# Kernel optimization log

Measured on AMD Instinct MI355X. Metric: run time of the kernel, lower is better.

The kernel has to match this reference:

```python
import jax, jax.numpy as jnp
import numpy as np

C_M, C_Z, C = 256, 128, 32
LN_EPS = 1e-5


def setup_inputs() -> dict:
    key = jax.random.key(0)
    ks = jax.random.split(key, 9)
    S, R = 128, 384  # N_seq, N_res
    m = jax.random.normal(ks[0], (S, R, C_M), dtype=jnp.float32)
    ln_g = jnp.ones((C_M,), jnp.float32)
    ln_b = jnp.zeros((C_M,), jnp.float32)
    w1 = jax.random.normal(ks[1], (C_M, C), jnp.float32) / np.sqrt(C_M)
    b1 = jnp.zeros((C,), jnp.float32)
    w2 = jax.random.normal(ks[2], (C_M, C), jnp.float32) / np.sqrt(C_M)
    b2 = jnp.zeros((C,), jnp.float32)
    w_out = jax.random.normal(ks[3], (C * C, C_Z), jnp.float32) / np.sqrt(C * C)
    b_out = jnp.zeros((C_Z,), jnp.float32)
    return {"m": m, "ln_g": ln_g, "ln_b": ln_b, "w1": w1, "b1": b1,
            "w2": w2, "b2": b2, "w_out": w_out, "b_out": b_out}


def reference(m, ln_g, ln_b, w1, b1, w2, b2, w_out, b_out):
    S, R, _ = m.shape
    # LayerNorm over c_m
    mu = jnp.mean(m, axis=-1, keepdims=True)
    var = jnp.var(m, axis=-1, keepdims=True)
    mn = (m - mu) * jax.lax.rsqrt(var + LN_EPS) * ln_g + ln_b
    a = mn @ w1 + b1  # (S, R, c)
    b = mn @ w2 + b2  # (S, R, c)
    # outer product summed over N_seq: out[i,j,x,y] = sum_s a[s,i,x] b[s,j,y]
    o = jnp.einsum('six,sjy->ijxy', a, b)  # (R, R, c, c)
    o = o.reshape(R, R, C * C) @ w_out + b_out  # (R, R, c_z)
    return o / S
```

## Files before the change

### kernel.cpp

```cpp
#include <hip/hip_runtime.h>
#include <hip/hip_bf16.h>

#define R_RES 384
#define S_SEQ 128
#define CM 256
#define CC 32
#define CZ 128

typedef __attribute__((ext_vector_type(8))) short bf16x8;
typedef __attribute__((ext_vector_type(4))) float f32x4;
typedef __attribute__((ext_vector_type(16))) float f32x16;
typedef __attribute__((ext_vector_type(4))) int i32x4;

__device__ __forceinline__ short tobf16(float f) {
    union { __hip_bfloat16 h; short s; } u;
    u.h = __float2bfloat16(f);
    return u.s;
}

__global__ void k_transpose_wout(const float* __restrict__ w_out, short* __restrict__ wbTf) {
    __shared__ float t[64][65];
    int k0 = blockIdx.x * 64;
    int z0 = blockIdx.y * 64;
    int tid = threadIdx.x;
    int c = tid & 63, rg = tid >> 6;
#pragma unroll
    for (int rr = 0; rr < 16; ++rr) {
        int kk = rg * 16 + rr;
        t[kk][c] = w_out[(size_t)(k0 + kk) * CZ + z0 + c];
    }
    __syncthreads();
#pragma unroll
    for (int l = 0; l < 2; ++l) {
        int id = l * 256 + tid;
        int f = id >> 6;
        int ksl = f >> 1, fzl = f & 1;
        int ln = id & 63;
        int zl = fzl * 32 + (ln & 31);
        int kl = ksl * 16 + (ln >> 5) * 8;
        bf16x8 pk;
#pragma unroll
        for (int j = 0; j < 8; ++j) pk[j] = tobf16(t[kl + j][zl]);
        size_t fz = blockIdx.y * 2 + fzl;
        size_t ks16 = blockIdx.x * 4 + ksl;
        *(bf16x8*)(wbTf + ((fz * 64 + ks16) * 64 + ln) * 8) = pk;
    }
}

__global__ void k_pack_w12(const float* __restrict__ w1, const float* __restrict__ w2,
                           short* __restrict__ wcT) {
    int idx = blockIdx.x * 256 + threadIdx.x;
    int k = idx >> 6, n = idx & 63;
    float v = (n < 32) ? w1[k * CC + n] : w2[k * CC + (n - 32)];
    wcT[n * CM + k] = tobf16(v);
}

__global__ __launch_bounds__(256) void k_ln_proj(
    const float* __restrict__ M, const float* __restrict__ ln_g, const float* __restrict__ ln_b,
    const float* __restrict__ b1, const float* __restrict__ b2,
    const short* __restrict__ wcT, short* __restrict__ aTf, short* __restrict__ bTf) {
    __shared__ short mnb[64 * 256];
    __shared__ short ab_s[2][32 * 72];
    int r = blockIdx.x >> 1;
    int s0 = (blockIdx.x & 1) * 64;
    int tid = threadIdx.x, lane = tid & 63, w = tid >> 6;
    int g = lane >> 4, r16 = lane & 15;
    float4 gv = *(const float4*)(ln_g + lane * 4);
    float4 bv = *(const float4*)(ln_b + lane * 4);
    for (int it = 0; it < 16; ++it) {
        int sl = it * 4 + w;
        float4 v = *(const float4*)(M + ((size_t)(s0 + sl) * R_RES + r) * CM + lane * 4);
        float sum = v.x + v.y + v.z + v.w;
        float sq = v.x * v.x + v.y * v.y + v.z * v.z + v.w * v.w;
#pragma unroll
        for (int off = 32; off; off >>= 1) {
            sum += __shfl_xor(sum, off);
            sq  += __shfl_xor(sq, off);
        }
        float mu = sum * (1.0f / 256.0f);
        float var = sq * (1.0f / 256.0f) - mu * mu;
        float rstd = rsqrtf(var + 1e-5f);
        short4 mnp;
        mnp.x = tobf16((v.x - mu) * rstd * gv.x + bv.x);
        mnp.y = tobf16((v.y - mu) * rstd * gv.y + bv.y);
        mnp.z = tobf16((v.z - mu) * rstd * gv.z + bv.z);
        mnp.w = tobf16((v.w - mu) * rstd * gv.w + bv.w);
        int byte = sl * 512 + lane * 8;
        byte ^= ((sl & 7) << 4);
        *(short4*)((char*)mnb + byte) = mnp;
    }
    __syncthreads();
    f32x4 acc[4] = {{0,0,0,0},{0,0,0,0},{0,0,0,0},{0,0,0,0}};
    int srow = w * 16 + r16;
#pragma unroll
    for (int ks = 0; ks < 8; ++ks) {
        int byte = srow * 512 + ks * 64 + g * 16;
        byte ^= ((srow & 7) << 4);
        bf16x8 af = *(const bf16x8*)((const char*)mnb + byte);
#pragma unroll
        for (int nt = 0; nt < 4; ++nt) {
            bf16x8 bf = *(const bf16x8*)(wcT + (nt * 16 + r16) * CM + ks * 32 + g * 8);
            acc[nt] = __builtin_amdgcn_mfma_f32_16x16x32_bf16(af, bf, acc[nt], 0, 0, 0);
        }
    }
#pragma unroll
    for (int nt = 0; nt < 4; ++nt) {
        int n = nt * 16 + r16;
        int x = n & 31, sel = n >> 5;
        float bias = sel ? b2[x] : b1[x];
#pragma unroll
        for (int rr = 0; rr < 4; ++rr) {
            int sl = w * 16 + g * 4 + rr;
            ab_s[sel][x * 72 + sl] = tobf16(acc[nt][rr] + bias);
        }
    }
    __syncthreads();
    int piece = tid >> 6;
    int fl = piece >> 1, kl = piece & 1;
    int ln = tid & 63;
    int x = fl * 16 + (ln & 15);
    int s_loc = kl * 32 + (ln >> 4) * 8;
    i32x4 va = *(const i32x4*)((const char*)ab_s[0] + (x * 72 + s_loc) * 2);
    i32x4 vb = *(const i32x4*)((const char*)ab_s[1] + (x * 72 + s_loc) * 2);
    size_t off = ((((size_t)r * 2 + fl) * 4 + (s0 >> 5) + kl) * 64 + ln) * 16;
    *(i32x4*)((char*)aTf + off) = va;
    *(i32x4*)((char*)bTf + off) = vb;
}

__global__ __launch_bounds__(512, 4) void k_opm(
    const short* __restrict__ aTf, const short* __restrict__ bTf,
    const short* __restrict__ wbTf, const float* __restrict__ b_out,
    float* __restrict__ out) {
    __shared__ __align__(16) char smem[65536];
    int tid = threadIdx.x, lane = tid & 63, w = tid >> 6;
    int g = lane >> 4, r16 = lane & 15;
    int l32 = lane & 31, h = lane >> 5;
    int wm = w & 3, wn = w >> 2;
    int bj = blockIdx.x, bi = blockIdx.y;

    const char* gB = (const char*)bTf + (size_t)bj * 32768;
#pragma unroll
    for (int it = 0; it < 4; ++it) {
        int q = it * 8192 + tid * 16;
        __builtin_amdgcn_global_load_lds(
            (const __attribute__((address_space(1))) void*)(gB + q),
            (__attribute__((address_space(3))) void*)(smem + q), 16, 0, 0);
    }
    __syncthreads();

    f32x4 acc[4][4] = {};
    const char* gA = (const char*)aTf + ((size_t)bi * 16 + wm * 4) * 4096;
#pragma unroll
    for (int ks = 0; ks < 4; ++ks) {
        bf16x8 bf[4], af[4];
#pragma unroll
        for (int ni = 0; ni < 4; ++ni)
            bf[ni] = *(const bf16x8*)(smem + (((wn * 4 + ni) * 4 + ks) * 64 + lane) * 16);
#pragma unroll
        for (int mi = 0; mi < 4; ++mi)
            af[mi] = *(const bf16x8*)(gA + ((mi * 4 + ks) * 64 + lane) * 16);
        __builtin_amdgcn_s_setprio(1);
#pragma unroll
        for (int mi = 0; mi < 4; ++mi)
#pragma unroll
            for (int ni = 0; ni < 4; ++ni)
                acc[mi][ni] = __builtin_amdgcn_mfma_f32_16x16x32_bf16(bf[ni], af[mi], acc[mi][ni], 0, 0, 0);
        __builtin_amdgcn_s_setprio(0);
    }
    __syncthreads();

#pragma unroll
    for (int mi = 0; mi < 4; ++mi)
#pragma unroll
        for (int ni = 0; ni < 4; ++ni) {
            int m = wm * 64 + mi * 16 + r16;
            int nb = wn * 64 + ni * 16 + g * 4;
            int i = m >> 5, x = m & 31;
            int j = nb >> 5, y0 = nb & 31;
            int p = i * 4 + j;
            int byte = (p * 2048 + x * 64 + y0 * 2) ^ (((p & 7) ^ (x & 7)) << 4);
            short4 pk;
            pk.x = tobf16(acc[mi][ni][0]);
            pk.y = tobf16(acc[mi][ni][1]);
            pk.z = tobf16(acc[mi][ni][2]);
            pk.w = tobf16(acc[mi][ni][3]);
            *(short4*)(smem + byte) = pk;
        }
    __syncthreads();

    int kh = w & 1, zq = w >> 1;
    f32x16 c2a = {0,0,0,0,0,0,0,0,0,0,0,0,0,0,0,0};
    f32x16 c2b = {0,0,0,0,0,0,0,0,0,0,0,0,0,0,0,0};
    const short* wbase = wbTf + (size_t)((zq * 64 + kh * 32) * 64) * 8;
#pragma unroll 8
    for (int ks = 0; ks < 32; ++ks) {
        int x = (kh * 32 + ks) >> 1;
        int byte = (l32 * 2048 + kh * 1024 + ks * 32 + h * 16) ^ ((((l32 & 7) ^ (x & 7))) << 4);
        bf16x8 a2f = *(const bf16x8*)(smem + byte);
        bf16x8 wbf = *(const bf16x8*)(wbase + (ks * 64 + lane) * 8);
        if (ks & 1) c2b = __builtin_amdgcn_mfma_f32_32x32x16_bf16(a2f, wbf, c2b, 0, 0, 0);
        else        c2a = __builtin_amdgcn_mfma_f32_32x32x16_bf16(a2f, wbf, c2a, 0, 0, 0);
    }
    f32x16 c2 = c2a + c2b;
    __syncthreads();

#pragma unroll
    for (int q = 0; q < 4; ++q) {
        f32x4 v;
        v[0] = c2[q * 4 + 0]; v[1] = c2[q * 4 + 1];
        v[2] = c2[q * 4 + 2]; v[3] = c2[q * 4 + 3];
        int byte = ((zq * 2 + kh) * 4096 + l32 * 128 + q * 32 + h * 16) ^ ((l32 & 7) << 4);
        *(f32x4*)(smem + byte) = v;
    }
    __syncthreads();

    int z = tid & 127, zq2 = z >> 5, zp = z & 31;
    int pr0 = tid >> 7;
    float bo = b_out[z];
#pragma unroll
    for (int stp = 0; stp < 2; ++stp) {
        int prq = pr0 + stp * 4;
        int base = zq2 * 8192 + zp * 128 + prq * 16;
        int sw = (zp & 7) << 4;
        f32x4 v0 = *(const f32x4*)(smem + (base ^ sw));
        f32x4 v1 = *(const f32x4*)(smem + ((base + 4096) ^ sw));
#pragma unroll
        for (int rr = 0; rr < 4; ++rr) {
            int p = prq * 4 + rr;
            int ig = bi * 8 + (p >> 2);
            int jg = bj * 4 + (p & 3);
            out[((size_t)ig * R_RES + jg) * CZ + z] = (v0[rr] + v1[rr] + bo) * (1.0f / 128.0f);
        }
    }
}

extern "C" void kernel_launch(void* const* d_in, const int* in_sizes, int n_in,
                              void* d_out, int out_size, void* d_ws, size_t ws_size,
                              hipStream_t stream) {
    const float* M     = (const float*)d_in[0];
    const float* ln_g  = (const float*)d_in[1];
    const float* ln_b  = (const float*)d_in[2];
    const float* w1    = (const float*)d_in[3];
    const float* b1    = (const float*)d_in[4];
    const float* w2    = (const float*)d_in[5];
    const float* b2    = (const float*)d_in[6];
    const float* w_out = (const float*)d_in[7];
    const float* b_out = (const float*)d_in[8];
    float* out = (float*)d_out;

    short* aTf  = (short*)d_ws;
    short* bTf  = aTf + 12288 * 128;
    short* wbTf = bTf + 12288 * 128;
    short* wcT  = wbTf + 128 * 1024;

    k_transpose_wout<<<dim3(16, 2), 256, 0, stream>>>(w_out, wbTf);
    k_pack_w12<<<64, 256, 0, stream>>>(w1, w2, wcT);
    k_ln_proj<<<768, 256, 0, stream>>>(M, ln_g, ln_b, b1, b2, wcT, aTf, bTf);
    k_opm<<<dim3(96, 48), 512, 0, stream>>>(aTf, bTf, wbTf, b_out, out);
}
```

Measured before the change: 133.8 us.

## Double outer-product block tile to 8x8 residue pairs with A staged in LDS

Each k_opm block now computes an 8x8 tile of residue pairs with 1024 threads and 128KB of LDS, instead of 8x4 with 512 threads. Both the A and B projections are staged into LDS with global_load_lds, so A is no longer read straight from global memory. Halving the block count halves the number of times the full W_out slice is streamed from L2 per output pair. The epilogue is also rewritten so each thread writes two vectorized float4 stores. The cost is a very large LDS footprint, likely one block per CU, and extra register pressure from the 1024-thread launch bounds.

Measured after the change: 143.6 us. +7.3%, slower.

```diff
diff --git a/kernel.cpp b/kernel.cpp
--- a/kernel.cpp
+++ b/kernel.cpp
@@ -127,38 +127,41 @@
     *(i32x4*)((char*)bTf + off) = vb;
 }
 
-__global__ __launch_bounds__(512, 4) void k_opm(
+__global__ __launch_bounds__(1024, 4) void k_opm(
     const short* __restrict__ aTf, const short* __restrict__ bTf,
     const short* __restrict__ wbTf, const float* __restrict__ b_out,
     float* __restrict__ out) {
-    __shared__ __align__(16) char smem[65536];
+    __shared__ __align__(16) char smem[131072];
     int tid = threadIdx.x, lane = tid & 63, w = tid >> 6;
     int g = lane >> 4, r16 = lane & 15;
     int l32 = lane & 31, h = lane >> 5;
     int wm = w & 3, wn = w >> 2;
     int bj = blockIdx.x, bi = blockIdx.y;
 
-    const char* gB = (const char*)bTf + (size_t)bj * 32768;
+    const char* gA = (const char*)aTf + (size_t)bi * 65536;
+    const char* gB = (const char*)bTf + (size_t)bj * 65536;
 #pragma unroll
     for (int it = 0; it < 4; ++it) {
-        int q = it * 8192 + tid * 16;
+        int q = it * 16384 + tid * 16;
+        __builtin_amdgcn_global_load_lds(
+            (const __attribute__((address_space(1))) void*)(gA + q),
+            (__attribute__((address_space(3))) void*)(smem + q), 16, 0, 0);
         __builtin_amdgcn_global_load_lds(
             (const __attribute__((address_space(1))) void*)(gB + q),
-            (__attribute__((address_space(3))) void*)(smem + q), 16, 0, 0);
+            (__attribute__((address_space(3))) void*)(smem + 65536 + q), 16, 0, 0);
     }
     __syncthreads();
 
     f32x4 acc[4][4] = {};
-    const char* gA = (const char*)aTf + ((size_t)bi * 16 + wm * 4) * 4096;
 #pragma unroll
     for (int ks = 0; ks < 4; ++ks) {
         bf16x8 bf[4], af[4];
 #pragma unroll
         for (int ni = 0; ni < 4; ++ni)
-            bf[ni] = *(const bf16x8*)(smem + (((wn * 4 + ni) * 4 + ks) * 64 + lane) * 16);
+            bf[ni] = *(const bf16x8*)(smem + 65536 + (((wn * 4 + ni) * 4 + ks) * 64 + lane) * 16);
 #pragma unroll
         for (int mi = 0; mi < 4; ++mi)
-            af[mi] = *(const bf16x8*)(gA + ((mi * 4 + ks) * 64 + lane) * 16);
+            af[mi] = *(const bf16x8*)(smem + (((wm * 4 + mi) * 4 + ks) * 64 + lane) * 16);
         __builtin_amdgcn_s_setprio(1);
 #pragma unroll
         for (int mi = 0; mi < 4; ++mi)
@@ -177,7 +180,7 @@
             int nb = wn * 64 + ni * 16 + g * 4;
             int i = m >> 5, x = m & 31;
             int j = nb >> 5, y0 = nb & 31;
-            int p = i * 4 + j;
+            int p = i * 8 + j;
             int byte = (p * 2048 + x * 64 + y0 * 2) ^ (((p & 7) ^ (x & 7)) << 4);
             short4 pk;
             pk.x = tobf16(acc[mi][ni][0]);
@@ -188,14 +191,16 @@
         }
     __syncthreads();
 
-    int kh = w & 1, zq = w >> 1;
+    int kh = w & 1, zq = (w >> 1) & 3, pd = w >> 3;
     f32x16 c2a = {0,0,0,0,0,0,0,0,0,0,0,0,0,0,0,0};
     f32x16 c2b = {0,0,0,0,0,0,0,0,0,0,0,0,0,0,0,0};
     const short* wbase = wbTf + (size_t)((zq * 64 + kh * 32) * 64) * 8;
+    int pbase = pd * 32 + l32;
 #pragma unroll 8
     for (int ks = 0; ks < 32; ++ks) {
-        int x = (kh * 32 + ks) >> 1;
-        int byte = (l32 * 2048 + kh * 1024 + ks * 32 + h * 16) ^ ((((l32 & 7) ^ (x & 7))) << 4);
+        int x = kh * 16 + (ks >> 1);
+        int byte = (pbase * 2048 + kh * 1024 + ks * 32 + h * 16)
+                   ^ ((((l32 & 7) ^ (x & 7))) << 4);
         bf16x8 a2f = *(const bf16x8*)(smem + byte);
         bf16x8 wbf = *(const bf16x8*)(wbase + (ks * 64 + lane) * 8);
         if (ks & 1) c2b = __builtin_amdgcn_mfma_f32_32x32x16_bf16(a2f, wbf, c2b, 0, 0, 0);
@@ -205,32 +210,41 @@
     __syncthreads();
 
 #pragma unroll
-    for (int q = 0; q < 4; ++q) {
-        f32x4 v;
-        v[0] = c2[q * 4 + 0]; v[1] = c2[q * 4 + 1];
-        v[2] = c2[q * 4 + 2]; v[3] = c2[q * 4 + 3];
-        int byte = ((zq * 2 + kh) * 4096 + l32 * 128 + q * 32 + h * 16) ^ ((l32 & 7) << 4);
-        *(f32x4*)(smem + byte) = v;
-    }
-    __syncthreads();
-
-    int z = tid & 127, zq2 = z >> 5, zp = z & 31;
-    int pr0 = tid >> 7;
-    float bo = b_out[z];
-#pragma unroll
-    for (int stp = 0; stp < 2; ++stp) {
-        int prq = pr0 + stp * 4;
-        int base = zq2 * 8192 + zp * 128 + prq * 16;
-        int sw = (zp & 7) << 4;
-        f32x4 v0 = *(const f32x4*)(smem + (base ^ sw));
-        f32x4 v1 = *(const f32x4*)(smem + ((base + 4096) ^ sw));
+    for (int q = 0; q < 4; ++q)
 #pragma unroll
         for (int rr = 0; rr < 4; ++rr) {
-            int p = prq * 4 + rr;
-            int ig = bi * 8 + (p >> 2);
-            int jg = bj * 4 + (p & 3);
-            out[((size_t)ig * R_RES + jg) * CZ + z] = (v0[rr] + v1[rr] + bo) * (1.0f / 128.0f);
-        }
+            int prow = pd * 32 + q * 8 + h * 4 + rr;
+            int zz = zq * 32 + l32;
+            int byte = (kh * 32768 + prow * 512 + zz * 4) ^ ((prow & 1) << 4);
+            *(float*)(smem + byte) = c2[q * 4 + rr];
+        }
+    __syncthreads();
+
+    {
+        int p = tid >> 4;
+        int zo = (tid & 15) * 8;
+        int sw = (p & 1) << 4;
+        int base = p * 512 + zo * 4;
+        f32x4 u0 = *(const f32x4*)(smem + ((base) ^ sw));
+        f32x4 u1 = *(const f32x4*)(smem + ((base + 16) ^ sw));
+        f32x4 v0 = *(const f32x4*)(smem + ((base + 32768) ^ sw));
+        f32x4 v1 = *(const f32x4*)(smem + ((base + 16 + 32768) ^ sw));
+        float4 bo0 = *(const float4*)(b_out + zo);
+        float4 bo1 = *(const float4*)(b_out + zo + 4);
+        f32x4 r0, r1;
+        r0[0] = (u0[0] + v0[0] + bo0.x) * (1.0f / 128.0f);
+        r0[1] = (u0[1] + v0[1] + bo0.y) * (1.0f / 128.0f);
+        r0[2] = (u0[2] + v0[2] + bo0.z) * (1.0f / 128.0f);
+        r0[3] = (u0[3] + v0[3] + bo0.w) * (1.0f / 128.0f);
+        r1[0] = (u1[0] + v1[0] + bo1.x) * (1.0f / 128.0f);
+        r1[1] = (u1[1] + v1[1] + bo1.y) * (1.0f / 128.0f);
+        r1[2] = (u1[2] + v1[2] + bo1.z) * (1.0f / 128.0f);
+        r1[3] = (u1[3] + v1[3] + bo1.w) * (1.0f / 128.0f);
+        int ig = bi * 8 + (p >> 3);
+        int jg = bj * 8 + (p & 7);
+        float* po = out + ((size_t)ig * R_RES + jg) * CZ + zo;
+        *(f32x4*)(po) = r0;
+        *(f32x4*)(po + 4) = r1;
     }
 }
 
@@ -256,5 +270,5 @@
     k_transpose_wout<<<dim3(16, 2), 256, 0, stream>>>(w_out, wbTf);
     k_pack_w12<<<64, 256, 0, stream>>>(w1, w2, wcT);
     k_ln_proj<<<768, 256, 0, stream>>>(M, ln_g, ln_b, b1, b2, wcT, aTf, bTf);
-    k_opm<<<dim3(96, 48), 512, 0, stream>>>(aTf, bTf, wbTf, b_out, out);
-}
+    k_opm<<<dim3(48, 48), 1024, 0, stream>>>(aTf, bTf, wbTf, b_out, out);
+}
```

## Remap OPM warp tiling, prefetch A and W fragments, use lgkm-only barriers

Applied to the files above, without the earlier changes.

The outer-product stage now has each warp own one full i row (2x8 MFMA tiles) instead of a 4x4 tile, so each warp reuses two A fragments across all eight B fragments. A fragments are prefetched one k-step ahead from global memory. W_out fragments for the second GEMM are software-pipelined four steps ahead, with their first loads issued before the barrier. The __syncthreads calls become lgkmcnt-only waits plus s_barrier, and one barrier between the accumulator dump and the second GEMM is merged with the prefetch. The gains depend on the compiler keeping outstanding vmem loads correctly ordered; register pressure also rises.

Result: faster. 128.1 us (-4.3%).

```diff
diff --git a/kernel.cpp b/kernel.cpp
--- a/kernel.cpp
+++ b/kernel.cpp
@@ -16,6 +16,12 @@
     union { __hip_bfloat16 h; short s; } u;
     u.h = __float2bfloat16(f);
     return u.s;
+}
+
+__device__ __forceinline__ void lgkm_barrier() {
+    asm volatile("s_waitcnt lgkmcnt(0)" ::: "memory");
+    __builtin_amdgcn_s_barrier();
+    __builtin_amdgcn_sched_barrier(0);
 }
 
 __global__ void k_transpose_wout(const float* __restrict__ w_out, short* __restrict__ wbTf) {
@@ -135,7 +141,7 @@
     int tid = threadIdx.x, lane = tid & 63, w = tid >> 6;
     int g = lane >> 4, r16 = lane & 15;
     int l32 = lane & 31, h = lane >> 5;
-    int wm = w & 3, wn = w >> 2;
+    int wm = w;
     int bj = blockIdx.x, bi = blockIdx.y;
 
     const char* gB = (const char*)bTf + (size_t)bj * 32768;
@@ -146,38 +152,51 @@
             (const __attribute__((address_space(1))) void*)(gB + q),
             (__attribute__((address_space(3))) void*)(smem + q), 16, 0, 0);
     }
-    __syncthreads();
-
-    f32x4 acc[4][4] = {};
-    const char* gA = (const char*)aTf + ((size_t)bi * 16 + wm * 4) * 4096;
+    const char* gA = (const char*)aTf + (size_t)bi * 65536;
+    bf16x8 afc0 = *(const bf16x8*)(gA + (((wm * 2 + 0) * 4 + 0) * 64 + lane) * 16);
+    bf16x8 afc1 = *(const bf16x8*)(gA + (((wm * 2 + 1) * 4 + 0) * 64 + lane) * 16);
+    __syncthreads();
+
+    f32x4 acc[2][8] = {};
 #pragma unroll
     for (int ks = 0; ks < 4; ++ks) {
-        bf16x8 bf[4], af[4];
+        int ksn = (ks + 1) & 3;
+        bf16x8 bf[8];
 #pragma unroll
         for (int ni = 0; ni < 4; ++ni)
-            bf[ni] = *(const bf16x8*)(smem + (((wn * 4 + ni) * 4 + ks) * 64 + lane) * 16);
-#pragma unroll
-        for (int mi = 0; mi < 4; ++mi)
-            af[mi] = *(const bf16x8*)(gA + ((mi * 4 + ks) * 64 + lane) * 16);
+            bf[ni] = *(const bf16x8*)(smem + ((ni * 4 + ks) * 64 + lane) * 16);
+        bf16x8 afn0 = *(const bf16x8*)(gA + (((wm * 2 + 0) * 4 + ksn) * 64 + lane) * 16);
+        bf16x8 afn1 = *(const bf16x8*)(gA + (((wm * 2 + 1) * 4 + ksn) * 64 + lane) * 16);
         __builtin_amdgcn_s_setprio(1);
 #pragma unroll
-        for (int mi = 0; mi < 4; ++mi)
-#pragma unroll
-            for (int ni = 0; ni < 4; ++ni)
-                acc[mi][ni] = __builtin_amdgcn_mfma_f32_16x16x32_bf16(bf[ni], af[mi], acc[mi][ni], 0, 0, 0);
+        for (int ni = 0; ni < 4; ++ni) {
+            acc[0][ni] = __builtin_amdgcn_mfma_f32_16x16x32_bf16(bf[ni], afc0, acc[0][ni], 0, 0, 0);
+            acc[1][ni] = __builtin_amdgcn_mfma_f32_16x16x32_bf16(bf[ni], afc1, acc[1][ni], 0, 0, 0);
+        }
         __builtin_amdgcn_s_setprio(0);
-    }
-    __syncthreads();
-
-#pragma unroll
-    for (int mi = 0; mi < 4; ++mi)
-#pragma unroll
-        for (int ni = 0; ni < 4; ++ni) {
-            int m = wm * 64 + mi * 16 + r16;
-            int nb = wn * 64 + ni * 16 + g * 4;
-            int i = m >> 5, x = m & 31;
+#pragma unroll
+        for (int ni = 4; ni < 8; ++ni)
+            bf[ni] = *(const bf16x8*)(smem + ((ni * 4 + ks) * 64 + lane) * 16);
+        __builtin_amdgcn_s_setprio(1);
+#pragma unroll
+        for (int ni = 4; ni < 8; ++ni) {
+            acc[0][ni] = __builtin_amdgcn_mfma_f32_16x16x32_bf16(bf[ni], afc0, acc[0][ni], 0, 0, 0);
+            acc[1][ni] = __builtin_amdgcn_mfma_f32_16x16x32_bf16(bf[ni], afc1, acc[1][ni], 0, 0, 0);
+        }
+        __builtin_amdgcn_s_setprio(0);
+        afc0 = afn0;
+        afc1 = afn1;
+    }
+    lgkm_barrier();
+
+#pragma unroll
+    for (int mi = 0; mi < 2; ++mi)
+#pragma unroll
+        for (int ni = 0; ni < 8; ++ni) {
+            int x = mi * 16 + r16;
+            int nb = ni * 16 + g * 4;
             int j = nb >> 5, y0 = nb & 31;
-            int p = i * 4 + j;
+            int p = wm * 4 + j;
             int byte = (p * 2048 + x * 64 + y0 * 2) ^ (((p & 7) ^ (x & 7)) << 4);
             short4 pk;
             pk.x = tobf16(acc[mi][ni][0]);
@@ -186,23 +205,43 @@
             pk.w = tobf16(acc[mi][ni][3]);
             *(short4*)(smem + byte) = pk;
         }
-    __syncthreads();
 
     int kh = w & 1, zq = w >> 1;
+    const short* wbase = wbTf + (size_t)((zq * 64 + kh * 32) * 64) * 8;
+    bf16x8 wpf[4];
+#pragma unroll
+    for (int u = 0; u < 4; ++u)
+        wpf[u] = *(const bf16x8*)(wbase + (u * 64 + lane) * 8);
+    lgkm_barrier();
+
     f32x16 c2a = {0,0,0,0,0,0,0,0,0,0,0,0,0,0,0,0};
     f32x16 c2b = {0,0,0,0,0,0,0,0,0,0,0,0,0,0,0,0};
-    const short* wbase = wbTf + (size_t)((zq * 64 + kh * 32) * 64) * 8;
-#pragma unroll 8
-    for (int ks = 0; ks < 32; ++ks) {
-        int x = (kh * 32 + ks) >> 1;
-        int byte = (l32 * 2048 + kh * 1024 + ks * 32 + h * 16) ^ ((((l32 & 7) ^ (x & 7))) << 4);
-        bf16x8 a2f = *(const bf16x8*)(smem + byte);
-        bf16x8 wbf = *(const bf16x8*)(wbase + (ks * 64 + lane) * 8);
-        if (ks & 1) c2b = __builtin_amdgcn_mfma_f32_32x32x16_bf16(a2f, wbf, c2b, 0, 0, 0);
-        else        c2a = __builtin_amdgcn_mfma_f32_32x32x16_bf16(a2f, wbf, c2a, 0, 0, 0);
+#pragma unroll
+    for (int kq = 0; kq < 8; ++kq) {
+        bf16x8 w0 = wpf[0], w1 = wpf[1], w2 = wpf[2], w3 = wpf[3];
+        if (kq < 7) {
+#pragma unroll
+            for (int u = 0; u < 4; ++u)
+                wpf[u] = *(const bf16x8*)(wbase + ((kq * 4 + 4 + u) * 64 + lane) * 8);
+        }
+        bf16x8 a2f[4];
+#pragma unroll
+        for (int u = 0; u < 4; ++u) {
+            int ks = kq * 4 + u;
+            int x = (kh * 32 + ks) >> 1;
+            int byte = (l32 * 2048 + kh * 1024 + ks * 32 + h * 16)
+                       ^ ((((l32 & 7) ^ (x & 7))) << 4);
+            a2f[u] = *(const bf16x8*)(smem + byte);
+        }
+        __builtin_amdgcn_s_setprio(1);
+        c2a = __builtin_amdgcn_mfma_f32_32x32x16_bf16(a2f[0], w0, c2a, 0, 0, 0);
+        c2b = __builtin_amdgcn_mfma_f32_32x32x16_bf16(a2f[1], w1, c2b, 0, 0, 0);
+        c2a = __builtin_amdgcn_mfma_f32_32x32x16_bf16(a2f[2], w2, c2a, 0, 0, 0);
+        c2b = __builtin_amdgcn_mfma_f32_32x32x16_bf16(a2f[3], w3, c2b, 0, 0, 0);
+        __builtin_amdgcn_s_setprio(0);
     }
     f32x16 c2 = c2a + c2b;
-    __syncthreads();
+    lgkm_barrier();
 
 #pragma unroll
     for (int q = 0; q < 4; ++q) {
@@ -212,7 +251,7 @@
         int byte = ((zq * 2 + kh) * 4096 + l32 * 128 + q * 32 + h * 16) ^ ((l32 & 7) << 4);
         *(f32x4*)(smem + byte) = v;
     }
-    __syncthreads();
+    lgkm_barrier();
 
     int z = tid & 127, zq2 = z >> 5, zp = z & 31;
     int pr0 = tid >> 7;
```

## Make OPM kernel persistent with register-resident w_out and prefetched B tiles

Applied to the files above, without the earlier changes.

Replaces the 96x48 grid with 512 persistent blocks that each process 18 output tiles of 4x4 residue pairs. Each block keeps its w_out slice in registers across all tiles. It prefetches the next B tile into LDS and the next A fragment while the current tile finishes. The w_out packing layout is changed to match 16x16x32 MFMAs in the second GEMM. The goal is to amortise weight loads and launch overhead and to overlap global loads with compute, at the cost of heavy register use (32 bf16x8 weights per thread), more LDS, and smaller per-tile work with extra barriers.

Measured after the change: 409.8 us. 3.06x slower.

```diff
diff --git a/kernel.cpp b/kernel.cpp
--- a/kernel.cpp
+++ b/kernel.cpp
@@ -9,13 +9,18 @@
 
 typedef __attribute__((ext_vector_type(8))) short bf16x8;
 typedef __attribute__((ext_vector_type(4))) float f32x4;
-typedef __attribute__((ext_vector_type(16))) float f32x16;
 typedef __attribute__((ext_vector_type(4))) int i32x4;
 
 __device__ __forceinline__ short tobf16(float f) {
     union { __hip_bfloat16 h; short s; } u;
     u.h = __float2bfloat16(f);
     return u.s;
+}
+
+__device__ __forceinline__ void lgkm_barrier() {
+    asm volatile("s_waitcnt lgkmcnt(0)" ::: "memory");
+    __builtin_amdgcn_s_barrier();
+    __builtin_amdgcn_sched_barrier(0);
 }
 
 __global__ void k_transpose_wout(const float* __restrict__ w_out, short* __restrict__ wbTf) {
@@ -34,16 +39,16 @@
     for (int l = 0; l < 2; ++l) {
         int id = l * 256 + tid;
         int f = id >> 6;
-        int ksl = f >> 1, fzl = f & 1;
+        int z16l = f >> 1, k32l = f & 1;
         int ln = id & 63;
-        int zl = fzl * 32 + (ln & 31);
-        int kl = ksl * 16 + (ln >> 5) * 8;
+        int zl = z16l * 16 + (ln & 15);
+        int kl = k32l * 32 + (ln >> 4) * 8;
         bf16x8 pk;
 #pragma unroll
         for (int j = 0; j < 8; ++j) pk[j] = tobf16(t[kl + j][zl]);
-        size_t fz = blockIdx.y * 2 + fzl;
-        size_t ks16 = blockIdx.x * 4 + ksl;
-        *(bf16x8*)(wbTf + ((fz * 64 + ks16) * 64 + ln) * 8) = pk;
+        int z16 = blockIdx.y * 4 + z16l;
+        int k32 = blockIdx.x * 2 + k32l;
+        *(bf16x8*)(wbTf + ((size_t)(z16 * 32 + k32) * 64 + ln) * 8) = pk;
     }
 }
 
@@ -131,106 +136,123 @@
     const short* __restrict__ aTf, const short* __restrict__ bTf,
     const short* __restrict__ wbTf, const float* __restrict__ b_out,
     float* __restrict__ out) {
-    __shared__ __align__(16) char smem[65536];
+    __shared__ __align__(16) char smem[81920];
     int tid = threadIdx.x, lane = tid & 63, w = tid >> 6;
     int g = lane >> 4, r16 = lane & 15;
-    int l32 = lane & 31, h = lane >> 5;
-    int wm = w & 3, wn = w >> 2;
-    int bj = blockIdx.x, bi = blockIdx.y;
-
-    const char* gB = (const char*)bTf + (size_t)bj * 32768;
-#pragma unroll
-    for (int it = 0; it < 4; ++it) {
-        int q = it * 8192 + tid * 16;
-        __builtin_amdgcn_global_load_lds(
-            (const __attribute__((address_space(1))) void*)(gB + q),
-            (__attribute__((address_space(3))) void*)(smem + q), 16, 0, 0);
-    }
-    __syncthreads();
-
-    f32x4 acc[4][4] = {};
-    const char* gA = (const char*)aTf + ((size_t)bi * 16 + wm * 4) * 4096;
-#pragma unroll
-    for (int ks = 0; ks < 4; ++ks) {
-        bf16x8 bf[4], af[4];
-#pragma unroll
-        for (int ni = 0; ni < 4; ++ni)
-            bf[ni] = *(const bf16x8*)(smem + (((wn * 4 + ni) * 4 + ks) * 64 + lane) * 16);
-#pragma unroll
-        for (int mi = 0; mi < 4; ++mi)
-            af[mi] = *(const bf16x8*)(gA + ((mi * 4 + ks) * 64 + lane) * 16);
-        __builtin_amdgcn_s_setprio(1);
-#pragma unroll
-        for (int mi = 0; mi < 4; ++mi)
-#pragma unroll
-            for (int ni = 0; ni < 4; ++ni)
-                acc[mi][ni] = __builtin_amdgcn_mfma_f32_16x16x32_bf16(bf[ni], af[mi], acc[mi][ni], 0, 0, 0);
-        __builtin_amdgcn_s_setprio(0);
-    }
-    __syncthreads();
-
-#pragma unroll
-    for (int mi = 0; mi < 4; ++mi)
-#pragma unroll
-        for (int ni = 0; ni < 4; ++ni) {
-            int m = wm * 64 + mi * 16 + r16;
-            int nb = wn * 64 + ni * 16 + g * 4;
-            int i = m >> 5, x = m & 31;
-            int j = nb >> 5, y0 = nb & 31;
-            int p = i * 4 + j;
+    int wm = w;
+    int kh = w & 1, zq = w >> 1;
+
+    bf16x8 wb[2][16];
+#pragma unroll
+    for (int zt = 0; zt < 2; ++zt)
+#pragma unroll
+        for (int ks2 = 0; ks2 < 16; ++ks2)
+            wb[zt][ks2] = *(const bf16x8*)(wbTf +
+                (((size_t)(zq * 2 + zt) * 32 + kh * 16 + ks2) * 64 + lane) * 8);
+
+    int pR = tid >> 5;
+    int zR = (tid & 31) * 4;
+    float4 bo4 = *(const float4*)(b_out + zR);
+
+    int t0 = blockIdx.x * 18;
+    const char* Ab = (const char*)aTf;
+    const char* Bb = (const char*)bTf;
+
+    {
+        const char* gB = Bb + (size_t)(t0 % 96) * 32768;
+#pragma unroll
+        for (int q = 0; q < 4; ++q)
+            __builtin_amdgcn_global_load_lds(
+                (const __attribute__((address_space(1))) void*)(gB + q * 8192 + tid * 16),
+                (__attribute__((address_space(3))) void*)(smem + q * 8192 + tid * 16), 16, 0, 0);
+    }
+    bf16x8 afc = *(const bf16x8*)(Ab + ((size_t)((t0 / 96) * 8 + wm) * 4 + 0) * 1024 + lane * 16);
+    asm volatile("s_waitcnt vmcnt(0)" ::: "memory");
+    __syncthreads();
+
+    for (int it = 0; it < 18; ++it) {
+        int t = t0 + it;
+        int bi = t / 96, bj = t % 96;
+        int tn = (it < 17) ? t + 1 : t0;
+        const char* gAc = Ab + (size_t)(bi * 8 + wm) * 4096;
+        const char* gAn = Ab + (size_t)((tn / 96) * 8 + wm) * 4096;
+
+        f32x4 acc[8] = {};
+#pragma unroll
+        for (int ks = 0; ks < 4; ++ks) {
+            bf16x8 bf[8];
+#pragma unroll
+            for (int ni = 0; ni < 8; ++ni)
+                bf[ni] = *(const bf16x8*)(smem + ((ni * 4 + ks) * 64 + lane) * 16);
+            bf16x8 afn = (ks < 3)
+                ? *(const bf16x8*)(gAc + (ks + 1) * 1024 + lane * 16)
+                : *(const bf16x8*)(gAn + lane * 16);
+            __builtin_amdgcn_s_setprio(1);
+#pragma unroll
+            for (int ni = 0; ni < 8; ++ni)
+                acc[ni] = __builtin_amdgcn_mfma_f32_16x16x32_bf16(bf[ni], afc, acc[ni], 0, 0, 0);
+            __builtin_amdgcn_s_setprio(0);
+            afc = afn;
+        }
+        lgkm_barrier();
+
+        if (it < 17) {
+            const char* gB = Bb + (size_t)(tn % 96) * 32768;
+#pragma unroll
+            for (int q = 0; q < 4; ++q)
+                __builtin_amdgcn_global_load_lds(
+                    (const __attribute__((address_space(1))) void*)(gB + q * 8192 + tid * 16),
+                    (__attribute__((address_space(3))) void*)(smem + q * 8192 + tid * 16), 16, 0, 0);
+        }
+
+#pragma unroll
+        for (int ni = 0; ni < 8; ++ni) {
+            int x = (wm & 1) * 16 + r16;
+            int p = (wm >> 1) * 4 + (ni >> 1);
+            int y0 = (ni & 1) * 16 + g * 4;
             int byte = (p * 2048 + x * 64 + y0 * 2) ^ (((p & 7) ^ (x & 7)) << 4);
             short4 pk;
-            pk.x = tobf16(acc[mi][ni][0]);
-            pk.y = tobf16(acc[mi][ni][1]);
-            pk.z = tobf16(acc[mi][ni][2]);
-            pk.w = tobf16(acc[mi][ni][3]);
-            *(short4*)(smem + byte) = pk;
-        }
-    __syncthreads();
-
-    int kh = w & 1, zq = w >> 1;
-    f32x16 c2a = {0,0,0,0,0,0,0,0,0,0,0,0,0,0,0,0};
-    f32x16 c2b = {0,0,0,0,0,0,0,0,0,0,0,0,0,0,0,0};
-    const short* wbase = wbTf + (size_t)((zq * 64 + kh * 32) * 64) * 8;
-#pragma unroll 8
-    for (int ks = 0; ks < 32; ++ks) {
-        int x = (kh * 32 + ks) >> 1;
-        int byte = (l32 * 2048 + kh * 1024 + ks * 32 + h * 16) ^ ((((l32 & 7) ^ (x & 7))) << 4);
-        bf16x8 a2f = *(const bf16x8*)(smem + byte);
-        bf16x8 wbf = *(const bf16x8*)(wbase + (ks * 64 + lane) * 8);
-        if (ks & 1) c2b = __builtin_amdgcn_mfma_f32_32x32x16_bf16(a2f, wbf, c2b, 0, 0, 0);
-        else        c2a = __builtin_amdgcn_mfma_f32_32x32x16_bf16(a2f, wbf, c2a, 0, 0, 0);
-    }
-    f32x16 c2 = c2a + c2b;
-    __syncthreads();
-
-#pragma unroll
-    for (int q = 0; q < 4; ++q) {
-        f32x4 v;
-        v[0] = c2[q * 4 + 0]; v[1] = c2[q * 4 + 1];
-        v[2] = c2[q * 4 + 2]; v[3] = c2[q * 4 + 3];
-        int byte = ((zq * 2 + kh) * 4096 + l32 * 128 + q * 32 + h * 16) ^ ((l32 & 7) << 4);
-        *(f32x4*)(smem + byte) = v;
-    }
-    __syncthreads();
-
-    int z = tid & 127, zq2 = z >> 5, zp = z & 31;
-    int pr0 = tid >> 7;
-    float bo = b_out[z];
-#pragma unroll
-    for (int stp = 0; stp < 2; ++stp) {
-        int prq = pr0 + stp * 4;
-        int base = zq2 * 8192 + zp * 128 + prq * 16;
-        int sw = (zp & 7) << 4;
-        f32x4 v0 = *(const f32x4*)(smem + (base ^ sw));
-        f32x4 v1 = *(const f32x4*)(smem + ((base + 4096) ^ sw));
-#pragma unroll
-        for (int rr = 0; rr < 4; ++rr) {
-            int p = prq * 4 + rr;
-            int ig = bi * 8 + (p >> 2);
-            int jg = bj * 4 + (p & 3);
-            out[((size_t)ig * R_RES + jg) * CZ + z] = (v0[rr] + v1[rr] + bo) * (1.0f / 128.0f);
-        }
+            pk.x = tobf16(acc[ni][0]);
+            pk.y = tobf16(acc[ni][1]);
+            pk.z = tobf16(acc[ni][2]);
+            pk.w = tobf16(acc[ni][3]);
+            *(short4*)(smem + 32768 + byte) = pk;
+        }
+        lgkm_barrier();
+
+        f32x4 c0 = {0,0,0,0}, c1 = {0,0,0,0};
+#pragma unroll
+        for (int ks2 = 0; ks2 < 16; ++ks2) {
+            int x = kh * 16 + ks2;
+            int abyte = (r16 * 2048 + x * 64 + g * 16) ^ ((((r16 & 7) ^ (x & 7))) << 4);
+            bf16x8 a2f = *(const bf16x8*)(smem + 32768 + abyte);
+            c0 = __builtin_amdgcn_mfma_f32_16x16x32_bf16(wb[0][ks2], a2f, c0, 0, 0, 0);
+            c1 = __builtin_amdgcn_mfma_f32_16x16x32_bf16(wb[1][ks2], a2f, c1, 0, 0, 0);
+        }
+        {
+            int b0 = (kh * 8192 + r16 * 512 + (zq * 32 + g * 4) * 4) ^ ((r16 & 7) << 4);
+            int b1 = (kh * 8192 + r16 * 512 + (zq * 32 + 16 + g * 4) * 4) ^ ((r16 & 7) << 4);
+            *(f32x4*)(smem + 65536 + b0) = c0;
+            *(f32x4*)(smem + 65536 + b1) = c1;
+        }
+        lgkm_barrier();
+
+        {
+            int base = (pR * 512 + zR * 4) ^ ((pR & 7) << 4);
+            f32x4 v0 = *(const f32x4*)(smem + 65536 + base);
+            f32x4 v1 = *(const f32x4*)(smem + 65536 + 8192 + base);
+            f32x4 res;
+            res[0] = (v0[0] + v1[0] + bo4.x) * (1.0f / 128.0f);
+            res[1] = (v0[1] + v1[1] + bo4.y) * (1.0f / 128.0f);
+            res[2] = (v0[2] + v1[2] + bo4.z) * (1.0f / 128.0f);
+            res[3] = (v0[3] + v1[3] + bo4.w) * (1.0f / 128.0f);
+            int ig = bi * 4 + (pR >> 2);
+            int jg = bj * 4 + (pR & 3);
+            *(f32x4*)(out + ((size_t)ig * R_RES + jg) * CZ + zR) = res;
+        }
+
+        asm volatile("s_waitcnt vmcnt(0)" ::: "memory");
+        __syncthreads();
     }
 }
 
@@ -256,5 +278,5 @@
     k_transpose_wout<<<dim3(16, 2), 256, 0, stream>>>(w_out, wbTf);
     k_pack_w12<<<64, 256, 0, stream>>>(w1, w2, wcT);
     k_ln_proj<<<768, 256, 0, stream>>>(M, ln_g, ln_b, b1, b2, wcT, aTf, bTf);
-    k_opm<<<dim3(96, 48), 512, 0, stream>>>(aTf, bTf, wbTf, b_out, out);
-}
+    k_opm<<<512, 512, 0, stream>>>(aTf, bTf, wbTf, b_out, out);
+}
```
